# Kernel optimization log

Hardware: AMD Instinct MI355X
Metric: run time of the kernel (lower is better)

The kernel has to match this reference:

```python
import jax, jax.numpy as jnp
import numpy as np

# pywt Wavelet('db4') decomposition filters (8 taps)
DEC_LO = jnp.array([-0.010597401784997278, 0.032883011666982945, 0.030841381835986965,
                    -0.18703481171888114, -0.02798376941698385, 0.6308807679295904,
                    0.7148465705525415, 0.23037781330885523], dtype=jnp.float32)
DEC_HI = jnp.array([-0.23037781330885523, 0.7148465705525415, -0.6308807679295904,
                    -0.02798376941698385, 0.18703481171888114, 0.030841381835986965,
                    -0.032883011666982945, -0.010597401784997278], dtype=jnp.float32)
FLEN = 8
LEVEL = 3


def _dwt_last(x, f):
    """Single-level DWT along last axis, pywt 'symmetric' mode.
    out[i] = sum_k f[k] * ext[2i+1-k] (true convolution, downsample by 2)."""
    p = FLEN - 1
    pad = [(0, 0)] * (x.ndim - 1) + [(p, p)]
    xp = jnp.pad(x, pad, mode='symmetric')[..., 1:]
    n = x.shape[-1]
    out_len = (n + FLEN - 1) // 2
    f_rev = f[::-1]
    y = f_rev[0] * xp[..., 0:2 * out_len:2]
    for j in range(1, FLEN):  # fixed 8-tap loop
        y = y + f_rev[j] * xp[..., j:j + 2 * out_len:2]
    return y


def _dwt_h(x, f):
    # DWT along axis -2 (rows/H)
    return jnp.swapaxes(_dwt_last(jnp.swapaxes(x, -1, -2), f), -1, -2)


def _dwt2(x):
    # x: [B, H, W] -> (cA, cH, cV, cD), matching pywt dwt2 ('aa','da','ad','dd')
    lo_w = _dwt_last(x, DEC_LO)
    hi_w = _dwt_last(x, DEC_HI)
    cA = _dwt_h(lo_w, DEC_LO)  # low H,  low W
    cH = _dwt_h(lo_w, DEC_HI)  # high H, low W  (horizontal detail)
    cV = _dwt_h(hi_w, DEC_LO)  # low H,  high W (vertical detail)
    cD = _dwt_h(hi_w, DEC_HI)  # high H, high W (diagonal detail)
    return cA, cH, cV, cD


def setup_inputs() -> dict:
    key = jax.random.key(0)
    x = jax.random.normal(key, (16, 1, 1024, 1024), dtype=jnp.float32)
    return {"x": x}


def reference(x):
    # wavedec2 ordering: (cA_L, (cH_L, cV_L, cD_L), ..., (cH_1, cV_1, cD_1))
    a = x[:, 0]  # [B, H, W]
    details = []
    for _ in range(LEVEL):
        a, lh, hl, hh = _dwt2(a)
        details.insert(0, (lh, hl, hh))  # coarsest first, as pywt returns
    outs = [a[:, None]]  # [B,1,h,w]
    for lh, hl, hh in details:
        outs += [lh[:, None], hl[:, None], hh[:, None]]
    return tuple(outs)
```

## Files before the change

### kernel.cpp

```cpp
#include <hip/hip_runtime.h>

__device__ __forceinline__ int refl(int i, int n) {
    i = (i < 0) ? (-i - 1) : i;
    i = (i >= n) ? (2 * n - 1 - i) : i;
    return i;
}

__device__ __forceinline__ unsigned bpack(float lo, float hi) {
    union { float f; unsigned u; } a, b;
    a.f = lo; b.f = hi;
    const unsigned ua = (a.u + 0x7FFFu + ((a.u >> 16) & 1u)) >> 16;
    const unsigned ub = (b.u + 0x7FFFu + ((b.u >> 16) & 1u)) & 0xFFFF0000u;
    return ua | ub;
}
__device__ __forceinline__ float b_lo(unsigned u) {
    union { unsigned u; float f; } x; x.u = u << 16; return x.f;
}
__device__ __forceinline__ float b_hi(unsigned u) {
    union { unsigned u; float f; } x; x.u = u & 0xFFFF0000u; return x.f;
}

__device__ __constant__ const float LOF[8] = {
    -0.010597401784997278f,  0.032883011666982945f,
     0.030841381835986965f, -0.18703481171888114f,
    -0.02798376941698385f,   0.6308807679295904f,
     0.7148465705525415f,    0.23037781330885523f };
__device__ __constant__ const float HIF[8] = {
    -0.23037781330885523f,   0.7148465705525415f,
    -0.6308807679295904f,   -0.02798376941698385f,
     0.18703481171888114f,   0.030841381835986965f,
    -0.032883011666982945f, -0.010597401784997278f };

template<int N, int LDIN, int M>
__global__ __launch_bounds__(256, 5)
void dwt_stripe(const float* __restrict__ in, int inb,
                float* __restrict__ oA, int ldA, int Ab,
                float* __restrict__ oH, float* __restrict__ oV,
                float* __restrict__ oD)
{
    constexpr int NG  = (M + 7) / 8;
    constexpr int LDP = 8 * NG;
    constexpr int S   = (M + 3) / 4;
    constexpr int NA  = 14 * NG;
    constexpr int NB  = 2 * LDP;

    __shared__ unsigned s[14 * LDP];

    const int G = gridDim.x;
    const int q = G >> 3, rm = G & 7;
    const int xcd = blockIdx.x & 7, pos = blockIdx.x >> 3;
    const int sid = xcd * q + (xcd < rm ? xcd : rm) + pos;
    const int sy = sid % S, b = sid / S;

    const int tid = threadIdx.x;
    const int gr0 = 4 * sy;
    const int rb  = 2 * gr0 - 6;
    const float* Ain = in + b * inb;

    #pragma unroll
    for (int k = 0; k < (NA + 255) / 256; ++k) {
        const int item = k * 256 + tid;
        if (item < NA) {
            const int trow = item / NG, g = item - trow * NG;
            const int ri = rb + trow;
            const int cb = 16 * g - 8;
            float v[24];
            if (ri >= 0 && ri < N && g >= 1 && 16 * g + 15 < N) {
                const float* p = Ain + ri * LDIN + cb;
                #pragma unroll
                for (int j = 0; j < 6; ++j) {
                    const float4 t4 = *(const float4*)(p + 4 * j);
                    v[4*j] = t4.x; v[4*j+1] = t4.y; v[4*j+2] = t4.z; v[4*j+3] = t4.w;
                }
            } else {
                const float* row = Ain + refl(ri, N) * LDIN;
                #pragma unroll
                for (int u = 0; u < 24; ++u) v[u] = row[refl(cb + u, N)];
            }
            unsigned w[8];
            #pragma unroll
            for (int d = 0; d < 8; ++d) {
                float lo = 0.f, hi = 0.f;
                #pragma unroll
                for (int t = 0; t < 8; ++t) {
                    const float x = v[2 * d + 9 - t];
                    lo += LOF[t] * x;
                    hi += HIF[t] * x;
                }
                w[d] = bpack(lo, hi);
            }
            unsigned* dst = &s[trow * LDP + 8 * g];
            *(uint4*)(dst)     = make_uint4(w[0], w[1], w[2], w[3]);
            *(uint4*)(dst + 4) = make_uint4(w[4], w[5], w[6], w[7]);
        }
    }
    __syncthreads();

    #pragma unroll
    for (int k = 0; k < (NB + 255) / 256; ++k) {
        const int item = k * 256 + tid;
        if (item < NB) {
            const int pr = item / LDP, c = item - pr * LDP;
            float lov[10], hiv[10];
            #pragma unroll
            for (int j = 0; j < 10; ++j) {
                const unsigned u = s[(4 * pr + j) * LDP + c];
                lov[j] = b_lo(u); hiv[j] = b_hi(u);
            }
            float A0 = 0.f, H0 = 0.f, V0 = 0.f, D0 = 0.f;
            float A1 = 0.f, H1 = 0.f, V1 = 0.f, D1 = 0.f;
            #pragma unroll
            for (int t = 0; t < 8; ++t) {
                const float l0 = lov[7 - t], h0 = hiv[7 - t];
                const float l1 = lov[9 - t], h1 = hiv[9 - t];
                A0 += LOF[t] * l0;  H0 += HIF[t] * l0;
                V0 += LOF[t] * h0;  D0 += HIF[t] * h0;
                A1 += LOF[t] * l1;  H1 += HIF[t] * l1;
                V1 += LOF[t] * h1;  D1 += HIF[t] * h1;
            }
            const int gr = gr0 + 2 * pr;
            if (c < M) {
                const int od = b * (M * M) + gr * M + c;
                if (gr < M) {
                    oA[b * Ab + gr * ldA + c] = A0;
                    oH[od] = H0; oV[od] = V0; oD[od] = D0;
                }
                if (gr + 1 < M) {
                    oA[b * Ab + (gr + 1) * ldA + c] = A1;
                    oH[od + M] = H1; oV[od + M] = V1; oD[od + M] = D1;
                }
            }
        }
    }
}

extern "C" void kernel_launch(void* const* d_in, const int* in_sizes, int n_in,
                              void* d_out, int out_size, void* d_ws, size_t ws_size,
                              hipStream_t stream) {
    const float* x = (const float*)d_in[0];
    float* out = (float*)d_out;
    float* ws  = (float*)d_ws;

    const int B = 16;
    const int m1 = 515, m2 = 261, m3 = 134;

    const int ld1 = 516, b1 = m1 * ld1;
    const int ld2 = 264, b2 = m2 * ld2;
    float* a1 = ws;
    float* a2 = ws + (size_t)b1 * B;

    const size_t sz1 = (size_t)B * m1 * m1;
    const size_t sz2 = (size_t)B * m2 * m2;
    const size_t sz3 = (size_t)B * m3 * m3;

    float* a3  = out;
    float* lh3 = a3  + sz3;
    float* hl3 = lh3 + sz3;
    float* hh3 = hl3 + sz3;
    float* lh2 = hh3 + sz3;
    float* hl2 = lh2 + sz2;
    float* hh2 = hl2 + sz2;
    float* lh1 = hh2 + sz2;
    float* hl1 = lh1 + sz1;
    float* hh1 = hl1 + sz1;

    const int S1 = (m1 + 3) / 4;
    const int S2 = (m2 + 3) / 4;
    const int S3 = (m3 + 3) / 4;

    dim3 blk(256);
    dwt_stripe<1024, 1024, 515><<<dim3(S1 * B), blk, 0, stream>>>(
        x, 1024 * 1024, a1, ld1, b1, lh1, hl1, hh1);
    dwt_stripe<515, 516, 261><<<dim3(S2 * B), blk, 0, stream>>>(
        a1, b1, a2, ld2, b2, lh2, hl2, hh2);
    dwt_stripe<261, 264, 134><<<dim3(S3 * B), blk, 0, stream>>>(
        a2, b2, a3, m3, m3 * m3, lh3, hl3, hh3);
}
```

Measured before the change: 59.59 us.

## Vectorize stripe column pass and use 2D tiled kernel for levels two and three

The first-level stripe kernel's second pass now has each thread handle four adjacent columns, reading uint4 from shared memory and writing float4 outputs, with a scalar path for the tail columns. Its launch-bounds occupancy hint drops from 5 to 3. Levels two and three switch to a new 32x32 2D-tiled kernel with 512 threads, which gives more blocks on the smaller images and uses a fast interior path. The float4 stores are unaligned, because the output row widths such as 515 are not multiples of four, and the tiles load overlapping halos again, which adds redundant reads.

```diff
diff --git a/kernel.cpp b/kernel.cpp
--- a/kernel.cpp
+++ b/kernel.cpp
@@ -1,4 +1,7 @@
 #include <hip/hip_runtime.h>
+
+typedef float f4 __attribute__((ext_vector_type(4)));
+typedef f4 f4u __attribute__((aligned(4)));
 
 __device__ __forceinline__ int refl(int i, int n) {
     i = (i < 0) ? (-i - 1) : i;
@@ -32,7 +35,7 @@
     -0.032883011666982945f, -0.010597401784997278f };
 
 template<int N, int LDIN, int M>
-__global__ __launch_bounds__(256, 5)
+__global__ __launch_bounds__(256, 3)
 void dwt_stripe(const float* __restrict__ in, int inb,
                 float* __restrict__ oA, int ldA, int Ab,
                 float* __restrict__ oH, float* __restrict__ oV,
@@ -42,7 +45,9 @@
     constexpr int LDP = 8 * NG;
     constexpr int S   = (M + 3) / 4;
     constexpr int NA  = 14 * NG;
-    constexpr int NB  = 2 * LDP;
+    constexpr int NQF = M / 4;
+    constexpr int TC  = M - 4 * NQF;
+    constexpr int NB  = 2 * NQF + 2 * TC;
 
     __shared__ unsigned s[14 * LDP];
 
@@ -99,16 +104,44 @@
     #pragma unroll
     for (int k = 0; k < (NB + 255) / 256; ++k) {
         const int item = k * 256 + tid;
-        if (item < NB) {
-            const int pr = item / LDP, c = item - pr * LDP;
+        if (item < 2 * NQF) {
+            const int pr = item / NQF, qc = item - pr * NQF;
+            uint4 qv[10];
+            #pragma unroll
+            for (int j = 0; j < 10; ++j)
+                qv[j] = *(const uint4*)&s[(4 * pr + j) * LDP + 4 * qc];
+
+            #pragma unroll
+            for (int d = 0; d < 2; ++d) {
+                const int gr = gr0 + 2 * pr + d;
+                if (gr >= M) continue;
+                f4 vA = 0.f, vH = 0.f, vV = 0.f, vD = 0.f;
+                #pragma unroll
+                for (int t = 0; t < 8; ++t) {
+                    const uint4 qq = qv[2 * d + 7 - t];
+                    f4 lo, hi;
+                    lo.x = b_lo(qq.x); lo.y = b_lo(qq.y); lo.z = b_lo(qq.z); lo.w = b_lo(qq.w);
+                    hi.x = b_hi(qq.x); hi.y = b_hi(qq.y); hi.z = b_hi(qq.z); hi.w = b_hi(qq.w);
+                    vA += LOF[t] * lo;  vH += HIF[t] * lo;
+                    vV += LOF[t] * hi;  vD += HIF[t] * hi;
+                }
+                const int cq = 4 * qc;
+                *(f4u*)&oA[b * Ab + gr * ldA + cq] = vA;
+                const int od = b * (M * M) + gr * M + cq;
+                *(f4u*)&oH[od] = vH;
+                *(f4u*)&oV[od] = vV;
+                *(f4u*)&oD[od] = vD;
+            }
+        } else if (item < NB) {
+            const int e = item - 2 * NQF;
+            const int pr = e & 1, c = 4 * NQF + (e >> 1);
             float lov[10], hiv[10];
             #pragma unroll
             for (int j = 0; j < 10; ++j) {
                 const unsigned u = s[(4 * pr + j) * LDP + c];
                 lov[j] = b_lo(u); hiv[j] = b_hi(u);
             }
-            float A0 = 0.f, H0 = 0.f, V0 = 0.f, D0 = 0.f;
-            float A1 = 0.f, H1 = 0.f, V1 = 0.f, D1 = 0.f;
+            float A0=0.f,H0=0.f,V0=0.f,D0=0.f,A1=0.f,H1=0.f,V1=0.f,D1=0.f;
             #pragma unroll
             for (int t = 0; t < 8; ++t) {
                 const float l0 = lov[7 - t], h0 = hiv[7 - t];
@@ -119,17 +152,145 @@
                 V1 += LOF[t] * h1;  D1 += HIF[t] * h1;
             }
             const int gr = gr0 + 2 * pr;
-            if (c < M) {
-                const int od = b * (M * M) + gr * M + c;
-                if (gr < M) {
-                    oA[b * Ab + gr * ldA + c] = A0;
-                    oH[od] = H0; oV[od] = V0; oD[od] = D0;
-                }
-                if (gr + 1 < M) {
-                    oA[b * Ab + (gr + 1) * ldA + c] = A1;
-                    oH[od + M] = H1; oV[od + M] = V1; oD[od + M] = D1;
-                }
-            }
+            const int od = b * (M * M) + gr * M + c;
+            if (gr < M) {
+                oA[b * Ab + gr * ldA + c] = A0;
+                oH[od] = H0; oV[od] = V0; oD[od] = D0;
+            }
+            if (gr + 1 < M) {
+                oA[b * Ab + (gr + 1) * ldA + c] = A1;
+                oH[od + M] = H1; oV[od + M] = V1; oD[od + M] = D1;
+            }
+        }
+    }
+}
+
+#define NTF 512
+__global__ __launch_bounds__(NTF, 8)
+void dwt2_fused(const float* __restrict__ in, int n, int ldin, int inb,
+                int m, int nty, int ntx,
+                float* __restrict__ oA, int ldA, int Ab,
+                float* __restrict__ oH, float* __restrict__ oV,
+                float* __restrict__ oD)
+{
+    __shared__ unsigned s[70 * 36];
+
+    const int G = gridDim.x;
+    const int q = G >> 3, rm = G & 7;
+    const int xcd = blockIdx.x & 7, pos = blockIdx.x >> 3;
+    const int i = xcd * q + (xcd < rm ? xcd : rm) + pos;
+    const int ty = i % nty;
+    const int t2 = i / nty;
+    const int tx = t2 % ntx;
+    const int b  = t2 / ntx;
+
+    const int tid = threadIdx.x;
+    const int c0 = tx * 32, r0 = ty * 32;
+    const float* Ain = in + b * inb;
+
+    const int rb  = 2 * r0 - 6;
+    const int cw0 = 2 * c0 - 8;
+    const bool interior = (rb >= 0) && (rb + 69 < n) && (cw0 >= 0) && (cw0 + 71 < n);
+
+    const int tr0 = tid >> 3, g0 = tid & 7;
+    const bool has2 = (tid < 48);
+    const int tr1 = 64 + (tid >> 3), g1 = tid & 7;
+
+    float v0[16], v1[16];
+    if (interior) {
+        const float* p0 = Ain + (rb + tr0) * ldin + (cw0 + 8 * g0);
+        const float4 a0 = ((const float4*)p0)[0];
+        const float4 a1 = ((const float4*)p0)[1];
+        const float4 a2 = ((const float4*)p0)[2];
+        const float4 a3 = ((const float4*)p0)[3];
+        v0[0]=a0.x; v0[1]=a0.y; v0[2]=a0.z; v0[3]=a0.w;
+        v0[4]=a1.x; v0[5]=a1.y; v0[6]=a1.z; v0[7]=a1.w;
+        v0[8]=a2.x; v0[9]=a2.y; v0[10]=a2.z; v0[11]=a2.w;
+        v0[12]=a3.x; v0[13]=a3.y; v0[14]=a3.z; v0[15]=a3.w;
+        if (has2) {
+            const float* p1 = Ain + (rb + tr1) * ldin + (cw0 + 8 * g1);
+            const float4 b0 = ((const float4*)p1)[0];
+            const float4 b1 = ((const float4*)p1)[1];
+            const float4 b2 = ((const float4*)p1)[2];
+            const float4 b3 = ((const float4*)p1)[3];
+            v1[0]=b0.x; v1[1]=b0.y; v1[2]=b0.z; v1[3]=b0.w;
+            v1[4]=b1.x; v1[5]=b1.y; v1[6]=b1.z; v1[7]=b1.w;
+            v1[8]=b2.x; v1[9]=b2.y; v1[10]=b2.z; v1[11]=b2.w;
+            v1[12]=b3.x; v1[13]=b3.y; v1[14]=b3.z; v1[15]=b3.w;
+        }
+    } else {
+        const float* row0 = Ain + refl(rb + tr0, n) * ldin;
+        const int cb0 = cw0 + 8 * g0;
+        #pragma unroll
+        for (int u = 0; u < 16; ++u) v0[u] = row0[refl(cb0 + u, n)];
+        if (has2) {
+            const float* row1 = Ain + refl(rb + tr1, n) * ldin;
+            const int cb1 = cw0 + 8 * g1;
+            #pragma unroll
+            for (int u = 0; u < 16; ++u) v1[u] = row1[refl(cb1 + u, n)];
+        }
+    }
+
+    {
+        unsigned w[4];
+        #pragma unroll
+        for (int d = 0; d < 4; ++d) {
+            float lo = 0.f, hi = 0.f;
+            #pragma unroll
+            for (int t = 0; t < 8; ++t) {
+                const float x = v0[2 * d + 9 - t];
+                lo += LOF[t] * x;
+                hi += HIF[t] * x;
+            }
+            w[d] = bpack(lo, hi);
+        }
+        *(uint4*)&s[tr0 * 36 + 4 * g0] = make_uint4(w[0], w[1], w[2], w[3]);
+    }
+    if (has2) {
+        unsigned w[4];
+        #pragma unroll
+        for (int d = 0; d < 4; ++d) {
+            float lo = 0.f, hi = 0.f;
+            #pragma unroll
+            for (int t = 0; t < 8; ++t) {
+                const float x = v1[2 * d + 9 - t];
+                lo += LOF[t] * x;
+                hi += HIF[t] * x;
+            }
+            w[d] = bpack(lo, hi);
+        }
+        *(uint4*)&s[tr1 * 36 + 4 * g1] = make_uint4(w[0], w[1], w[2], w[3]);
+    }
+    __syncthreads();
+
+    const int c = tid & 31, pr = tid >> 5;
+    float lov[10], hiv[10];
+    #pragma unroll
+    for (int j = 0; j < 10; ++j) {
+        const unsigned u = s[(4 * pr + j) * 36 + c];
+        lov[j] = b_lo(u); hiv[j] = b_hi(u);
+    }
+    float A0=0.f,H0=0.f,V0=0.f,D0=0.f,A1=0.f,H1=0.f,V1=0.f,D1=0.f;
+    #pragma unroll
+    for (int t = 0; t < 8; ++t) {
+        const float l0 = lov[7 - t], h0 = hiv[7 - t];
+        const float l1 = lov[9 - t], h1 = hiv[9 - t];
+        A0 += LOF[t] * l0;  H0 += HIF[t] * l0;
+        V0 += LOF[t] * h0;  D0 += HIF[t] * h0;
+        A1 += LOF[t] * l1;  H1 += HIF[t] * l1;
+        V1 += LOF[t] * h1;  D1 += HIF[t] * h1;
+    }
+    const int gr = r0 + 2 * pr, gc = c0 + c;
+    if (gc < m) {
+        const int ob = b * (m * m);
+        const int od = ob + gr * m + gc;
+        if (gr < m) {
+            oA[b * Ab + gr * ldA + gc] = A0;
+            oH[od] = H0; oV[od] = V0; oD[od] = D0;
+        }
+        if (gr + 1 < m) {
+            oA[b * Ab + (gr + 1) * ldA + gc] = A1;
+            oH[od + m] = H1; oV[od + m] = V1; oD[od + m] = D1;
         }
     }
 }
@@ -143,6 +304,7 @@
 
     const int B = 16;
     const int m1 = 515, m2 = 261, m3 = 134;
+    const int n2 = 515, n3 = 261;
 
     const int ld1 = 516, b1 = m1 * ld1;
     const int ld2 = 264, b2 = m2 * ld2;
@@ -165,14 +327,18 @@
     float* hh1 = hl1 + sz1;
 
     const int S1 = (m1 + 3) / 4;
-    const int S2 = (m2 + 3) / 4;
-    const int S3 = (m3 + 3) / 4;
+    const int t2_ = (m2 + 31) / 32;
+    const int t3  = (m3 + 31) / 32;
 
     dim3 blk(256);
     dwt_stripe<1024, 1024, 515><<<dim3(S1 * B), blk, 0, stream>>>(
         x, 1024 * 1024, a1, ld1, b1, lh1, hl1, hh1);
-    dwt_stripe<515, 516, 261><<<dim3(S2 * B), blk, 0, stream>>>(
-        a1, b1, a2, ld2, b2, lh2, hl2, hh2);
-    dwt_stripe<261, 264, 134><<<dim3(S3 * B), blk, 0, stream>>>(
-        a2, b2, a3, m3, m3 * m3, lh3, hl3, hh3);
-}
+
+    dwt2_fused<<<dim3(t2_ * t2_ * B), dim3(NTF), 0, stream>>>(
+        a1, n2, ld1, b1, m2, t2_, t2_,
+        a2, ld2, b2, lh2, hl2, hh2);
+
+    dwt2_fused<<<dim3(t3 * t3 * B), dim3(NTF), 0, stream>>>(
+        a2, n3, ld2, b2, m3, t3, t3,
+        a3, m3, m3 * m3, lh3, hl3, hh3);
+}
```

Result: faster. 56.75 us (-4.8%).
